# Performance work log

Measured on AMD Instinct MI355X. Metric: run time of the kernel, lower is better.

## Reference

```python
import jax, jax.numpy as jnp
import numpy as np


def setup_inputs() -> dict:
    key = jax.random.key(0)
    ks = jax.random.split(key, 5)
    b, n_q, n_kv = 16, 128, 4096
    query_dim, context_dim, heads, dim_head = 1024, 1024, 16, 64
    inner = heads * dim_head
    x = jax.random.normal(ks[0], (b, n_q, query_dim), dtype=jnp.float32)
    context = jax.random.normal(ks[1], (b, n_kv, context_dim), dtype=jnp.float32)
    # Linear weights stored as (in, out); scaled like default torch init magnitude
    Wq = jax.random.normal(ks[2], (query_dim, inner), dtype=jnp.float32) * (query_dim ** -0.5)
    Wkv = jax.random.normal(ks[3], (context_dim, 2 * inner), dtype=jnp.float32) * (context_dim ** -0.5)
    Wout = jax.random.normal(ks[4], (inner, query_dim), dtype=jnp.float32) * (inner ** -0.5)
    bout = jnp.zeros((query_dim,), dtype=jnp.float32)
    return {"x": x, "context": context, "Wq": Wq, "Wkv": Wkv, "Wout": Wout, "bout": bout}


def reference(x, context, Wq, Wkv, Wout, bout):
    heads, dim_head = 16, 64
    b, n_q, _ = x.shape
    n_kv = context.shape[1]
    scale = dim_head ** -0.5

    q = x @ Wq                       # [b, n_q, h*d]
    kv = context @ Wkv               # [b, n_kv, 2*h*d]
    k, v = jnp.split(kv, 2, axis=-1)

    def split_heads(t):
        bb, n, _ = t.shape
        return t.reshape(bb, n, heads, dim_head).transpose(0, 2, 1, 3)  # [b, h, n, d]

    q, k, v = map(split_heads, (q, k, v))

    # mask[i, j] = (i - (j % n_q) == 0)  -> query i attends keys j with j % n_q == i
    i_idx = jnp.arange(n_q)[:, None]
    j_idx = jnp.arange(n_kv)[None, :]
    mask = (j_idx % n_q) == i_idx      # [n_q, n_kv] bool

    sim = jnp.einsum('bhid,bhjd->bhij', q, k) * scale
    max_neg = -jnp.finfo(sim.dtype).max
    sim = jnp.where(mask[None, None, :, :], sim, max_neg)
    attn = jax.nn.softmax(sim, axis=-1)
    out = jnp.einsum('bhij,bhjd->bhid', attn, v)   # [b, h, n_q, d]
    out = out.transpose(0, 2, 1, 3).reshape(b, n_q, heads * dim_head)
    return out @ Wout + bout
```

## Files before the change

kernel.cpp:

```cpp
#include <hip/hip_runtime.h>
#include <hip/hip_bf16.h>

typedef __attribute__((ext_vector_type(8))) short short8;
typedef __attribute__((ext_vector_type(4))) float floatx4;

__device__ __forceinline__ unsigned short f32_to_bf16(float f) {
    unsigned int u = __builtin_bit_cast(unsigned int, f);
    u = (u + 0x7FFFu + ((u >> 16) & 1u)) >> 16;
    return (unsigned short)u;
}
__device__ __forceinline__ unsigned int pack_bf16x2(float lo, float hi) {
    return (unsigned int)f32_to_bf16(lo) | ((unsigned int)f32_to_bf16(hi) << 16);
}
__device__ __forceinline__ void async_load16(const unsigned short* g, unsigned short* l) {
    __builtin_amdgcn_global_load_lds(
        (const __attribute__((address_space(1))) void*)g,
        (__attribute__((address_space(3))) void*)l, 16, 0, 0);
}

__device__ __forceinline__ void transpose_tile(
    const float* __restrict__ W, int src_ld, int n_off,
    unsigned short* __restrict__ Wt, int dst_ld, int nb, int kb, int tid) {
    __shared__ float tile[32][33];
    int n0 = nb * 32, k0 = kb * 32;
    int tx = tid & 31, ty = tid >> 5;
#pragma unroll
    for (int p = 0; p < 4; ++p) {
        int r = ty + 8 * p;
        tile[r][tx] = W[(long)(k0 + r) * src_ld + n_off + n0 + tx];
    }
    __syncthreads();
#pragma unroll
    for (int p = 0; p < 4; ++p) {
        int r = ty + 8 * p;
        Wt[(long)(n0 + r) * dst_ld + k0 + tx] = f32_to_bf16(tile[tx][r]);
    }
}

__device__ __forceinline__ void cast8(
    const float* __restrict__ src, unsigned short* __restrict__ dst) {
    float4 a = *(const float4*)src;
    float4 b = *(const float4*)(src + 4);
    uint4 p;
    p.x = pack_bf16x2(a.x, a.y); p.y = pack_bf16x2(a.z, a.w);
    p.z = pack_bf16x2(b.x, b.y); p.w = pack_bf16x2(b.z, b.w);
    *(uint4*)dst = p;
}

__global__ __launch_bounds__(256) void prep_kernel(
    const float* __restrict__ Wq, const float* __restrict__ Wkv,
    const float* __restrict__ Wout, const float* __restrict__ x,
    unsigned short* __restrict__ WqT, unsigned short* __restrict__ WkB,
    unsigned short* __restrict__ WvT, unsigned short* __restrict__ WoutT,
    unsigned short* __restrict__ xb) {
    int id = blockIdx.x, tid = threadIdx.x;
    if (id < 1024) { transpose_tile(Wq,   1024, 0,    WqT,   1024, id & 31, id >> 5, tid); return; }
    id -= 1024;
    if (id < 1024) { transpose_tile(Wkv,  2048, 1024, WvT,   1024, id & 31, id >> 5, tid); return; }
    id -= 1024;
    if (id < 1024) { transpose_tile(Wout, 1024, 0,    WoutT, 1024, id & 31, id >> 5, tid); return; }
    id -= 1024;
    if (id < 512) {
        long e = ((long)id * 256 + tid) * 8;
        long row = e >> 10, col = e & 1023;
        cast8(Wkv + row * 2048 + col, WkB + e);
        return;
    }
    id -= 512;
    { long e = ((long)id * 256 + tid) * 8; cast8(x + e, xb + e); }
}

__global__ __launch_bounds__(256, 4) void gemm64_kernel(
    const unsigned short* __restrict__ A, long sA, int lda,
    const unsigned short* __restrict__ Bt, long sB, int ldb,
    void* __restrict__ C, long sC, int ldc,
    const float* __restrict__ bias, int K, int out_bf16) {
    __shared__ unsigned short As[128 * 32];
    __shared__ unsigned short Bs[64 * 32];

    const int tid = threadIdx.x, wave = tid >> 6, lane = tid & 63;
    const int z = blockIdx.z;
    A  += (long)z * sA;
    Bt += (long)z * sB;
    const int m0 = blockIdx.y * 128, n0 = blockIdx.x * 64;

    floatx4 acc[2][4];
#pragma unroll
    for (int i = 0; i < 2; ++i)
#pragma unroll
        for (int j = 0; j < 4; ++j) acc[i][j] = (floatx4)0.0f;

    const int kofs = (lane & 3) * 8;
    const unsigned short* aAddr = A  + (long)(m0 + wave * 32 + (lane >> 2)) * lda + kofs;
    const unsigned short* bAddr = Bt + (long)(n0 + wave * 16 + (lane >> 2)) * ldb + kofs;
    unsigned short* asBase = &As[wave * 1024];
    unsigned short* bsBase = &Bs[wave * 512];

    const int frm = lane & 15, fk = (lane >> 4) * 8;

    for (int kk = 0; kk < K; kk += 32) {
        __syncthreads();
        async_load16(aAddr + kk,                  asBase);
        async_load16(aAddr + (long)16 * lda + kk, asBase + 512);
        async_load16(bAddr + kk,                  bsBase);
        __syncthreads();

        short8 afrag[2], bfrag[4];
#pragma unroll
        for (int rt = 0; rt < 2; ++rt)
            afrag[rt] = *(const short8*)&As[(wave * 32 + rt * 16 + frm) * 32 + fk];
#pragma unroll
        for (int ct = 0; ct < 4; ++ct)
            bfrag[ct] = *(const short8*)&Bs[(ct * 16 + frm) * 32 + fk];
#pragma unroll
        for (int rt = 0; rt < 2; ++rt)
#pragma unroll
            for (int ct = 0; ct < 4; ++ct)
                acc[rt][ct] = __builtin_amdgcn_mfma_f32_16x16x32_bf16(
                    afrag[rt], bfrag[ct], acc[rt][ct], 0, 0, 0);
    }

    const int orow0 = m0 + wave * 32 + (lane >> 4) * 4;
    const int ocol0 = n0 + (lane & 15);
    if (out_bf16) {
        unsigned short* Cb = (unsigned short*)C + (long)z * sC;
#pragma unroll
        for (int rt = 0; rt < 2; ++rt)
#pragma unroll
            for (int r = 0; r < 4; ++r) {
                long row = orow0 + rt * 16 + r;
#pragma unroll
                for (int ct = 0; ct < 4; ++ct)
                    Cb[row * ldc + ocol0 + ct * 16] = f32_to_bf16(acc[rt][ct][r]);
            }
    } else {
        float* Cf = (float*)C + (long)z * sC;
#pragma unroll
        for (int rt = 0; rt < 2; ++rt)
#pragma unroll
            for (int r = 0; r < 4; ++r) {
                long row = orow0 + rt * 16 + r;
#pragma unroll
                for (int ct = 0; ct < 4; ++ct) {
                    int col = ocol0 + ct * 16;
                    float v = acc[rt][ct][r];
                    if (bias) v += bias[col];
                    Cf[row * ldc + col] = v;
                }
            }
    }
}

__global__ __launch_bounds__(256, 4) void gemm64s_kernel(
    const unsigned short* __restrict__ A, long sA, int lda,
    const unsigned short* __restrict__ Bt, long sB, int ldb,
    void* __restrict__ C, long sC, int ldc,
    const float* __restrict__ bias, int K, int out_bf16) {
    __shared__ unsigned short As[64 * 32];
    __shared__ unsigned short Bs[64 * 32];

    const int tid = threadIdx.x, wave = tid >> 6, lane = tid & 63;
    const int z = blockIdx.z;
    A  += (long)z * sA;
    Bt += (long)z * sB;
    const int m0 = blockIdx.y * 64, n0 = blockIdx.x * 64;

    floatx4 acc[4];
#pragma unroll
    for (int j = 0; j < 4; ++j) acc[j] = (floatx4)0.0f;

    const int kofs = (lane & 3) * 8;
    const unsigned short* aAddr = A  + (long)(m0 + wave * 16 + (lane >> 2)) * lda + kofs;
    const unsigned short* bAddr = Bt + (long)(n0 + wave * 16 + (lane >> 2)) * ldb + kofs;
    unsigned short* asBase = &As[wave * 512];
    unsigned short* bsBase = &Bs[wave * 512];

    const int frm = lane & 15, fk = (lane >> 4) * 8;

    for (int kk = 0; kk < K; kk += 32) {
        __syncthreads();
        async_load16(aAddr + kk, asBase);
        async_load16(bAddr + kk, bsBase);
        __syncthreads();

        short8 afrag = *(const short8*)&As[(wave * 16 + frm) * 32 + fk];
        short8 bfrag[4];
#pragma unroll
        for (int ct = 0; ct < 4; ++ct)
            bfrag[ct] = *(const short8*)&Bs[(ct * 16 + frm) * 32 + fk];
#pragma unroll
        for (int ct = 0; ct < 4; ++ct)
            acc[ct] = __builtin_amdgcn_mfma_f32_16x16x32_bf16(
                afrag, bfrag[ct], acc[ct], 0, 0, 0);
    }

    const int orow0 = m0 + wave * 16 + (lane >> 4) * 4;
    const int ocol0 = n0 + (lane & 15);
    if (out_bf16) {
        unsigned short* Cb = (unsigned short*)C + (long)z * sC;
#pragma unroll
        for (int r = 0; r < 4; ++r) {
            long row = orow0 + r;
#pragma unroll
            for (int ct = 0; ct < 4; ++ct)
                Cb[row * ldc + ocol0 + ct * 16] = f32_to_bf16(acc[ct][r]);
        }
    } else {
        float* Cf = (float*)C + (long)z * sC;
#pragma unroll
        for (int r = 0; r < 4; ++r) {
            long row = orow0 + r;
#pragma unroll
            for (int ct = 0; ct < 4; ++ct) {
                int col = ocol0 + ct * 16;
                float v = acc[ct][r];
                if (bias) v += bias[col];
                Cf[row * ldc + col] = v;
            }
        }
    }
}

#define CLD 1032
__global__ __launch_bounds__(256, 2) void attn_fused_kernel(
    const float* __restrict__ ctx,
    const unsigned short* __restrict__ qt,
    unsigned short* __restrict__ wctx) {
    __shared__ unsigned short ctx_t[32 * CLD];
    __shared__ float sred[4 * 512];
    __shared__ float s_f[512];
    __shared__ float mxs[16], inv_[16];
    __shared__ unsigned short p_l[16 * 40];

    const int tid = threadIdx.x, wave = tid >> 6, lane = tid & 63;
    const int bi = blockIdx.x;
    const int b = bi >> 7, i = bi & 127;
    const int frm = lane & 15, fk = (lane >> 4) * 8;

    short8 af[8];
    const unsigned short* qbase =
        qt + (long)bi * 16384 + (long)frm * 1024 + wave * 256 + fk;
#pragma unroll
    for (int it = 0; it < 8; ++it) af[it] = *(const short8*)(qbase + it * 32);

#pragma unroll
    for (int rr = 0; rr < 16; ++rr) {
        int idx = rr * 2048 + tid * 8;
        int t = idx >> 10, c = idx & 1023;
        cast8(ctx + ((long)b * 4096 + i + t * 128) * 1024 + c, &ctx_t[t * CLD + c]);
    }
    __syncthreads();

    floatx4 acc0 = (floatx4)0.0f, acc1 = (floatx4)0.0f;
#pragma unroll
    for (int it = 0; it < 8; ++it) {
        int kk = wave * 256 + it * 32;
        short8 b0 = *(const short8*)&ctx_t[frm * CLD + kk + fk];
        short8 b1 = *(const short8*)&ctx_t[(16 + frm) * CLD + kk + fk];
        acc0 = __builtin_amdgcn_mfma_f32_16x16x32_bf16(af[it], b0, acc0, 0, 0, 0);
        acc1 = __builtin_amdgcn_mfma_f32_16x16x32_bf16(af[it], b1, acc1, 0, 0, 0);
    }
#pragma unroll
    for (int r = 0; r < 4; ++r) {
        sred[wave * 512 + frm * 16 + (lane >> 4) * 4 + r]        = acc0[r];
        sred[wave * 512 + (16 + frm) * 16 + (lane >> 4) * 4 + r] = acc1[r];
    }
    __syncthreads();
#pragma unroll
    for (int half = 0; half < 2; ++half) {
        int idx = half * 256 + tid;
        s_f[idx] = (sred[idx] + sred[512 + idx] + sred[1024 + idx] + sred[1536 + idx]) * 0.125f;
    }
    __syncthreads();
    if (tid < 16) {
        int h = tid;
        float m = -1e30f;
        for (int t = 0; t < 32; ++t) m = fmaxf(m, s_f[t * 16 + h]);
        float den = 0.0f;
        for (int t = 0; t < 32; ++t) den += __expf(s_f[t * 16 + h] - m);
        mxs[h] = m; inv_[h] = 1.0f / den;
    }
    __syncthreads();
#pragma unroll
    for (int half = 0; half < 2; ++half) {
        int idx = half * 256 + tid;
        int t = idx >> 4, h = idx & 15;
        p_l[h * 40 + t] = f32_to_bf16(__expf(s_f[idx] - mxs[h]) * inv_[h]);
    }
    __syncthreads();

    short8 ap;
#pragma unroll
    for (int j = 0; j < 8; ++j) ap[j] = (short)p_l[frm * 40 + fk + j];
#pragma unroll 4
    for (int nt = 0; nt < 16; ++nt) {
        int c0 = wave * 256 + nt * 16;
        short8 bt;
#pragma unroll
        for (int j = 0; j < 8; ++j) bt[j] = (short)ctx_t[(fk + j) * CLD + c0 + frm];
        floatx4 wacc = __builtin_amdgcn_mfma_f32_16x16x32_bf16(ap, bt, (floatx4)0.0f, 0, 0, 0);
#pragma unroll
        for (int r = 0; r < 4; ++r) {
            int h = (lane >> 4) * 4 + r;
            wctx[(long)bi * 16384 + (long)h * 1024 + c0 + frm] = f32_to_bf16(wacc[r]);
        }
    }
}

extern "C" void kernel_launch(void* const* d_in, const int* in_sizes, int n_in,
                              void* d_out, int out_size, void* d_ws, size_t ws_size,
                              hipStream_t stream) {
    const float* x       = (const float*)d_in[0];
    const float* context = (const float*)d_in[1];
    const float* Wq      = (const float*)d_in[2];
    const float* Wkv     = (const float*)d_in[3];
    const float* Wout    = (const float*)d_in[4];
    const float* bout    = (const float*)d_in[5];
    float* out = (float*)d_out;

    char* ws = (char*)d_ws;
    unsigned short* WqT   = (unsigned short*)(ws);
    unsigned short* WkB   = (unsigned short*)(ws + (2ll  << 20));
    unsigned short* WvT   = (unsigned short*)(ws + (4ll  << 20));
    unsigned short* WoutT = (unsigned short*)(ws + (6ll  << 20));
    unsigned short* xb    = (unsigned short*)(ws + (8ll  << 20));
    unsigned short* qb    = (unsigned short*)(ws + (12ll << 20));
    unsigned short* aob   = (unsigned short*)(ws + (16ll << 20));
    unsigned short* qtb   = (unsigned short*)(ws + (32ll << 20));
    unsigned short* wctxb = (unsigned short*)(ws + (96ll << 20));

    prep_kernel<<<4608, 256, 0, stream>>>(Wq, Wkv, Wout, x, WqT, WkB, WvT, WoutT, xb);

    gemm64s_kernel<<<dim3(16, 32, 1), 256, 0, stream>>>(
        xb, 0, 1024, WqT, 0, 1024, qb, 0, 1024, nullptr, 1024, 1);
    gemm64_kernel<<<dim3(16, 16, 16), 256, 0, stream>>>(
        qb, 64, 1024, WkB, 64, 1024, qtb, 1024, 16384, nullptr, 64, 1);
    attn_fused_kernel<<<2048, 256, 0, stream>>>(context, qtb, wctxb);
    gemm64s_kernel<<<dim3(1, 32, 16), 256, 0, stream>>>(
        wctxb, 1024, 16384, WvT, (long)64 * 1024, 1024, aob, 64, 1024, nullptr, 1024, 1);
    gemm64s_kernel<<<dim3(16, 32, 1), 256, 0, stream>>>(
        aob, 0, 1024, WoutT, 0, 1024, out, 0, 1024, bout, 1024, 0);
}
```

Before: 471.6 us.

## Swizzle context LDS tile, warp-shuffle softmax, vectorized transposed wctx stores

Reworks the fused attention kernel. Context rows go into LDS with an XOR swizzle, and the reduction buffer is padded, both to cut bank conflicts. The 16-thread serial softmax becomes a per-wave shuffle reduction, which removes two barriers. The P·ctx MFMA operands are swapped so each lane writes four contiguous bf16 outputs as one 8-byte store. It also adds nontemporal loads for context and raises wave priority (setprio) around the MFMA loops, at the cost of more complex indexing.

After: 454.0 us. -3.7%, faster.

```diff
diff --git a/kernel.cpp b/kernel.cpp
--- a/kernel.cpp
+++ b/kernel.cpp
@@ -39,11 +39,21 @@
 
 __device__ __forceinline__ void cast8(
     const float* __restrict__ src, unsigned short* __restrict__ dst) {
-    float4 a = *(const float4*)src;
-    float4 b = *(const float4*)(src + 4);
+    floatx4 a = *(const floatx4*)src;
+    floatx4 b = *(const floatx4*)(src + 4);
     uint4 p;
-    p.x = pack_bf16x2(a.x, a.y); p.y = pack_bf16x2(a.z, a.w);
-    p.z = pack_bf16x2(b.x, b.y); p.w = pack_bf16x2(b.z, b.w);
+    p.x = pack_bf16x2(a[0], a[1]); p.y = pack_bf16x2(a[2], a[3]);
+    p.z = pack_bf16x2(b[0], b[1]); p.w = pack_bf16x2(b[2], b[3]);
+    *(uint4*)dst = p;
+}
+
+__device__ __forceinline__ void cast8_nt(
+    const float* __restrict__ src, unsigned short* __restrict__ dst) {
+    floatx4 a = __builtin_nontemporal_load((const floatx4*)src);
+    floatx4 b = __builtin_nontemporal_load((const floatx4*)(src + 4));
+    uint4 p;
+    p.x = pack_bf16x2(a[0], a[1]); p.y = pack_bf16x2(a[2], a[3]);
+    p.z = pack_bf16x2(b[0], b[1]); p.w = pack_bf16x2(b[2], b[3]);
     *(uint4*)dst = p;
 }
 
@@ -222,14 +232,15 @@
 }
 
 #define CLD 1032
+__device__ __forceinline__ int swzb(int t, int c) {
+    return t * (2 * CLD) + ((2 * c) ^ (((t >> 3) & 3) << 5));
+}
 __global__ __launch_bounds__(256, 2) void attn_fused_kernel(
     const float* __restrict__ ctx,
     const unsigned short* __restrict__ qt,
     unsigned short* __restrict__ wctx) {
     __shared__ unsigned short ctx_t[32 * CLD];
-    __shared__ float sred[4 * 512];
-    __shared__ float s_f[512];
-    __shared__ float mxs[16], inv_[16];
+    __shared__ float sred[4 * 544];
     __shared__ unsigned short p_l[16 * 40];
 
     const int tid = threadIdx.x, wave = tid >> 6, lane = tid & 63;
@@ -247,64 +258,71 @@
     for (int rr = 0; rr < 16; ++rr) {
         int idx = rr * 2048 + tid * 8;
         int t = idx >> 10, c = idx & 1023;
-        cast8(ctx + ((long)b * 4096 + i + t * 128) * 1024 + c, &ctx_t[t * CLD + c]);
+        cast8_nt(ctx + ((long)b * 4096 + i + t * 128) * 1024 + c,
+                 (unsigned short*)((char*)ctx_t + swzb(t, c)));
     }
     __syncthreads();
 
     floatx4 acc0 = (floatx4)0.0f, acc1 = (floatx4)0.0f;
+    __builtin_amdgcn_s_setprio(1);
 #pragma unroll
     for (int it = 0; it < 8; ++it) {
         int kk = wave * 256 + it * 32;
-        short8 b0 = *(const short8*)&ctx_t[frm * CLD + kk + fk];
-        short8 b1 = *(const short8*)&ctx_t[(16 + frm) * CLD + kk + fk];
+        short8 b0 = *(const short8*)((const char*)ctx_t + swzb(frm, kk + fk));
+        short8 b1 = *(const short8*)((const char*)ctx_t + swzb(16 + frm, kk + fk));
         acc0 = __builtin_amdgcn_mfma_f32_16x16x32_bf16(af[it], b0, acc0, 0, 0, 0);
         acc1 = __builtin_amdgcn_mfma_f32_16x16x32_bf16(af[it], b1, acc1, 0, 0, 0);
     }
+    __builtin_amdgcn_s_setprio(0);
 #pragma unroll
     for (int r = 0; r < 4; ++r) {
-        sred[wave * 512 + frm * 16 + (lane >> 4) * 4 + r]        = acc0[r];
-        sred[wave * 512 + (16 + frm) * 16 + (lane >> 4) * 4 + r] = acc1[r];
+        sred[wave * 544 + frm * 17 + (lane >> 4) * 4 + r]        = acc0[r];
+        sred[wave * 544 + (16 + frm) * 17 + (lane >> 4) * 4 + r] = acc1[r];
     }
     __syncthreads();
-#pragma unroll
-    for (int half = 0; half < 2; ++half) {
-        int idx = half * 256 + tid;
-        s_f[idx] = (sred[idx] + sred[512 + idx] + sred[1024 + idx] + sred[1536 + idx]) * 0.125f;
+
+    {
+        const int h = wave * 4 + (lane >> 4);
+        const int tg = lane & 15;
+        const int i0 = tg * 17 + h, i1 = (16 + tg) * 17 + h;
+        float s0 = (sred[i0] + sred[544 + i0] + sred[1088 + i0] + sred[1632 + i0]) * 0.125f;
+        float s1 = (sred[i1] + sred[544 + i1] + sred[1088 + i1] + sred[1632 + i1]) * 0.125f;
+        float m = fmaxf(s0, s1);
+#pragma unroll
+        for (int d = 1; d < 16; d <<= 1) m = fmaxf(m, __shfl_xor(m, d));
+        float e0 = __expf(s0 - m), e1 = __expf(s1 - m);
+        float den = e0 + e1;
+#pragma unroll
+        for (int d = 1; d < 16; d <<= 1) den += __shfl_xor(den, d);
+        float inv = 1.0f / den;
+        p_l[h * 40 + tg]      = f32_to_bf16(e0 * inv);
+        p_l[h * 40 + 16 + tg] = f32_to_bf16(e1 * inv);
     }
     __syncthreads();
-    if (tid < 16) {
-        int h = tid;
-        float m = -1e30f;
-        for (int t = 0; t < 32; ++t) m = fmaxf(m, s_f[t * 16 + h]);
-        float den = 0.0f;
-        for (int t = 0; t < 32; ++t) den += __expf(s_f[t * 16 + h] - m);
-        mxs[h] = m; inv_[h] = 1.0f / den;
-    }
-    __syncthreads();
-#pragma unroll
-    for (int half = 0; half < 2; ++half) {
-        int idx = half * 256 + tid;
-        int t = idx >> 4, h = idx & 15;
-        p_l[h * 40 + t] = f32_to_bf16(__expf(s_f[idx] - mxs[h]) * inv_[h]);
-    }
-    __syncthreads();
 
     short8 ap;
 #pragma unroll
     for (int j = 0; j < 8; ++j) ap[j] = (short)p_l[frm * 40 + fk + j];
+
+    unsigned short* wbase =
+        wctx + (long)bi * 16384 + (long)frm * 1024 + (lane >> 4) * 4;
+    __builtin_amdgcn_s_setprio(1);
 #pragma unroll 4
     for (int nt = 0; nt < 16; ++nt) {
         int c0 = wave * 256 + nt * 16;
-        short8 bt;
-#pragma unroll
-        for (int j = 0; j < 8; ++j) bt[j] = (short)ctx_t[(fk + j) * CLD + c0 + frm];
-        floatx4 wacc = __builtin_amdgcn_mfma_f32_16x16x32_bf16(ap, bt, (floatx4)0.0f, 0, 0, 0);
-#pragma unroll
-        for (int r = 0; r < 4; ++r) {
-            int h = (lane >> 4) * 4 + r;
-            wctx[(long)bi * 16384 + (long)h * 1024 + c0 + frm] = f32_to_bf16(wacc[r]);
-        }
-    }
+        short8 av;
+#pragma unroll
+        for (int j = 0; j < 8; ++j)
+            av[j] = (short)*(const unsigned short*)
+                        ((const char*)ctx_t + swzb(fk + j, c0 + frm));
+        floatx4 wacc = __builtin_amdgcn_mfma_f32_16x16x32_bf16(
+            av, ap, (floatx4)0.0f, 0, 0, 0);
+        uint2 st;
+        st.x = pack_bf16x2(wacc[0], wacc[1]);
+        st.y = pack_bf16x2(wacc[2], wacc[3]);
+        *(uint2*)(wbase + c0) = st;
+    }
+    __builtin_amdgcn_s_setprio(0);
 }
 
 extern "C" void kernel_launch(void* const* d_in, const int* in_sizes, int n_in,
```
